# Performance work log

Hardware: AMD Instinct MI355X
Metric: run time of the kernel (lower is better)

## Reference

```python
import jax, jax.numpy as jnp
import numpy as np

B, LQ, C = 4, 4096, 384
NH, NL, NP = 6, 1, 4
HL, WL = 64, 64
LV = HL * WL
DH = C // NH
EPS = 1e-6


def layer_norm(x, g, b):
    mu = jnp.mean(x, axis=-1, keepdims=True)
    var = jnp.mean(jnp.square(x - mu), axis=-1, keepdims=True)
    return (x - mu) * jax.lax.rsqrt(var + EPS) * g + b


def ms_deform_attn_core(value, spatial_shapes, level_start_index, loc, attn_w):
    # value [B,LV,NH,DH]; loc [B,LQ,NH,NL,NP,2] in [0,1]; attn_w [B,LQ,NH,NL,NP]
    ss = np.asarray(spatial_shapes)
    lsi = np.asarray(level_start_index)
    Bv, _, nH, dh = value.shape
    Lq = loc.shape[1]
    nP = loc.shape[4]
    out = jnp.zeros((Bv, Lq, nH, dh), value.dtype)
    for l in range(loc.shape[3]):
        Hl, Wl = int(ss[l, 0]), int(ss[l, 1])
        st = int(lsi[l])
        vflat = value[:, st:st + Hl * Wl]  # [B, Hl*Wl, nH, dh]
        xy = loc[:, :, :, l]               # [B,LQ,nH,NP,2]
        # grid_sample(align_corners=False): pixel = loc * size - 0.5
        x = xy[..., 0] * Wl - 0.5
        y = xy[..., 1] * Hl - 0.5
        x0 = jnp.floor(x)
        y0 = jnp.floor(y)
        wx = x - x0
        wy = y - y0
        x0i = x0.astype(jnp.int32)
        y0i = y0.astype(jnp.int32)

        def gather(xi, yi):
            # zero padding outside the feature map (padding_mode='zeros')
            valid = (xi >= 0) & (xi < Wl) & (yi >= 0) & (yi < Hl)
            idx = jnp.clip(yi, 0, Hl - 1) * Wl + jnp.clip(xi, 0, Wl - 1)  # [B,LQ,nH,NP]
            idx2 = idx.transpose(0, 1, 3, 2).reshape(Bv, Lq * nP, nH)
            g = jnp.take_along_axis(vflat, idx2[..., None], axis=1)       # [B,LQ*NP,nH,dh]
            g = g.reshape(Bv, Lq, nP, nH, dh).transpose(0, 1, 3, 2, 4)    # [B,LQ,nH,NP,dh]
            return g * valid[..., None].astype(value.dtype)

        samp = (gather(x0i, y0i) * ((1 - wx) * (1 - wy))[..., None]
                + gather(x0i + 1, y0i) * (wx * (1 - wy))[..., None]
                + gather(x0i, y0i + 1) * ((1 - wx) * wy)[..., None]
                + gather(x0i + 1, y0i + 1) * (wx * wy)[..., None])
        out = out + jnp.einsum('bqhpd,bqhp->bqhd', samp, attn_w[:, :, :, l])
    return out.reshape(Bv, Lq, nH * dh)


def setup_inputs() -> dict:
    key = jax.random.key(0)
    ks = jax.random.split(key, 12)
    s = 0.02
    return {
        'query': jax.random.normal(ks[0], (B, LQ, C), jnp.float32),
        'reference_points': jax.random.uniform(ks[1], (B, LQ, NL, 2), dtype=jnp.float32),
        'feat': jax.random.normal(ks[2], (B, LV, C), jnp.float32),
        'spatial_shapes': jnp.array([[HL, WL]], jnp.int32),
        'level_start_index': jnp.array([0], jnp.int32),
        'ln_q_g': jnp.ones((C,), jnp.float32), 'ln_q_b': jnp.zeros((C,), jnp.float32),
        'ln_f_g': jnp.ones((C,), jnp.float32), 'ln_f_b': jnp.zeros((C,), jnp.float32),
        'gamma': jax.random.normal(ks[3], (C,), jnp.float32) * 0.1,
        'Wv': jax.random.normal(ks[4], (C, C), jnp.float32) * s,
        'bv': jnp.zeros((C,), jnp.float32),
        'Wo': jax.random.normal(ks[5], (C, NH * NL * NP * 2), jnp.float32) * s,
        'bo': jax.random.normal(ks[6], (NH * NL * NP * 2,), jnp.float32) * 0.5,
        'Wa': jax.random.normal(ks[7], (C, NH * NL * NP), jnp.float32) * s,
        'ba': jnp.zeros((NH * NL * NP,), jnp.float32),
        'Wout': jax.random.normal(ks[8], (C, C), jnp.float32) * s,
        'bout': jnp.zeros((C,), jnp.float32),
    }


def reference(query, reference_points, feat, spatial_shapes, level_start_index,
              ln_q_g, ln_q_b, ln_f_g, ln_f_b, gamma,
              Wv, bv, Wo, bo, Wa, ba, Wout, bout):
    q = layer_norm(query, ln_q_g, ln_q_b)
    f = layer_norm(feat, ln_f_g, ln_f_b)
    value = (f @ Wv + bv).reshape(B, LV, NH, DH)
    offsets = (q @ Wo + bo).reshape(B, LQ, NH, NL, NP, 2)
    attn_w = jax.nn.softmax((q @ Wa + ba).reshape(B, LQ, NH, NL * NP), axis=-1)
    attn_w = attn_w.reshape(B, LQ, NH, NL, NP)
    # offset normalizer is (W, H) per level
    norm = jnp.stack([spatial_shapes[:, 1], spatial_shapes[:, 0]], -1).astype(jnp.float32)
    loc = reference_points[:, :, None, :, None, :] + offsets / norm[None, None, None, :, None, :]
    attn = ms_deform_attn_core(value, spatial_shapes, level_start_index, loc, attn_w)
    attn = attn @ Wout + bout
    return query + gamma * attn
```

## Files before the change

### kernel.cpp

```cpp
#include <hip/hip_runtime.h>
#include <math.h>

#define B_    4
#define LQ_   4096
#define C_    384
#define NH_   6
#define NP_   4
#define HL_   64
#define WL_   64
#define LV_   (HL_ * WL_)
#define ROWS_ (B_ * LQ_)
#define EPS_  1e-6f
#define NOFF_ 48
#define NLOG_ 24
#define WCTR_ 96

typedef unsigned short u16;
typedef unsigned int   u32;
typedef __bf16 bf16x8 __attribute__((ext_vector_type(8)));
typedef float  f32x4  __attribute__((ext_vector_type(4)));

__device__ __forceinline__ u16 f2bf(float f) {
    u32 u = __float_as_uint(f);
    u += 0x7fff + ((u >> 16) & 1);
    return (u16)(u >> 16);
}
__device__ __forceinline__ u32 pack2bf(float a, float b) {
    return (u32)f2bf(a) | ((u32)f2bf(b) << 16);
}

__device__ __forceinline__ f32x4 mfma16(bf16x8 a, bf16x8 b, f32x4 c) {
    return __builtin_amdgcn_mfma_f32_16x16x32_bf16(a, b, c, 0, 0, 0);
}

__device__ __forceinline__ void gl_lds16(const u16* g, u16* l) {
    __builtin_amdgcn_global_load_lds(
        (const __attribute__((address_space(1))) unsigned int*)g,
        (__attribute__((address_space(3))) unsigned int*)l, 16, 0, 0);
}

__device__ __forceinline__ void vm_wait8() { asm volatile("s_waitcnt vmcnt(8)" ::: "memory"); }
__device__ __forceinline__ void vm_wait7() { asm volatile("s_waitcnt vmcnt(7)" ::: "memory"); }
__device__ __forceinline__ void vm_wait6() { asm volatile("s_waitcnt vmcnt(6)" ::: "memory"); }
__device__ __forceinline__ void vm_wait0() { asm volatile("s_waitcnt vmcnt(0)" ::: "memory"); }
__device__ __forceinline__ void lgkm0()    { asm volatile("s_waitcnt lgkmcnt(0)" ::: "memory"); }
__device__ __forceinline__ void barrier_() { asm volatile("s_barrier" ::: "memory"); }

#define LN_BLOCKS_   8192
#define PREP_BLOCKS_ 1297

__global__ __launch_bounds__(256) void ln_prep(
    const float* __restrict__ query, const float* __restrict__ feat,
    const float* __restrict__ qg, const float* __restrict__ qbv,
    const float* __restrict__ fg, const float* __restrict__ fbv,
    u16* __restrict__ qout, u16* __restrict__ fout,
    const float* __restrict__ Wv, const float* __restrict__ Wout,
    const float* __restrict__ Wo, const float* __restrict__ Wa,
    const float* __restrict__ bo, const float* __restrict__ ba,
    u16* __restrict__ WvT, u16* __restrict__ WoutT, u16* __restrict__ WcT,
    float* __restrict__ bias_c)
{
    if (blockIdx.x < LN_BLOCKS_) {
        int wid  = threadIdx.x >> 6;
        int lane = threadIdx.x & 63;
        int row  = blockIdx.x * 4 + wid;
        const float *src, *g, *bsh;
        u16* dst;
        int r;
        if (row < ROWS_) { src = query; g = qg; bsh = qbv; dst = qout; r = row; }
        else             { src = feat;  g = fg; bsh = fbv; dst = fout; r = row - ROWS_; }

        const float* x = src + (size_t)r * C_;
        float4 a4 = *(const float4*)(x + 4 * lane);
        float2 a2 = *(const float2*)(x + 256 + 2 * lane);
        float v0 = a4.x, v1 = a4.y, v2 = a4.z, v3 = a4.w, v4 = a2.x, v5 = a2.y;

        float s = v0 + v1 + v2 + v3 + v4 + v5;
#pragma unroll
        for (int off = 32; off; off >>= 1) s += __shfl_xor(s, off);
        float mu = s * (1.f / C_);

        float d0 = v0 - mu, d1 = v1 - mu, d2 = v2 - mu;
        float d3 = v3 - mu, d4 = v4 - mu, d5 = v5 - mu;
        float s2 = d0*d0 + d1*d1 + d2*d2 + d3*d3 + d4*d4 + d5*d5;
#pragma unroll
        for (int off = 32; off; off >>= 1) s2 += __shfl_xor(s2, off);
        float rs = rsqrtf(s2 * (1.f / C_) + EPS_);

        float4 g4 = *(const float4*)(g + 4 * lane);
        float4 b4 = *(const float4*)(bsh + 4 * lane);
        float2 g2 = *(const float2*)(g + 256 + 2 * lane);
        float2 b2 = *(const float2*)(bsh + 256 + 2 * lane);

        float o0 = d0 * rs * g4.x + b4.x;
        float o1 = d1 * rs * g4.y + b4.y;
        float o2 = d2 * rs * g4.z + b4.z;
        float o3 = d3 * rs * g4.w + b4.w;
        float o4 = d4 * rs * g2.x + b2.x;
        float o5 = d5 * rs * g2.y + b2.y;

        u16* y = dst + (size_t)r * C_;
        uint2 w0; w0.x = pack2bf(o0, o1); w0.y = pack2bf(o2, o3);
        *(uint2*)(y + 4 * lane) = w0;
        *(u32*)(y + 256 + 2 * lane) = pack2bf(o4, o5);
    } else {
        const int KN = 384 * 384;
        int idx = (blockIdx.x - LN_BLOCKS_) * 256 + threadIdx.x;
        if (idx < KN) {
            int n = idx / 384, k = idx - n * 384;
            WvT[idx] = f2bf(Wv[k * 384 + n]);
        } else if (idx < 2 * KN) {
            int t = idx - KN;
            int n = t / 384, k = t - n * 384;
            WoutT[t] = f2bf(Wout[k * 384 + n]);
        } else if (idx < 2 * KN + WCTR_ * 384) {
            int t = idx - 2 * KN;
            int n = t / 384, k = t - n * 384;
            float v = (n < 48) ? Wo[k * 48 + n] : (n < 72 ? Wa[k * 24 + (n - 48)] : 0.f);
            WcT[t] = f2bf(v);
        } else if (idx < 2 * KN + WCTR_ * 384 + 80) {
            int n = idx - (2 * KN + WCTR_ * 384);
            bias_c[n] = (n < 48) ? bo[n] : (n < 72 ? ba[n - 48] : 0.f);
        }
    }
}

__global__ __launch_bounds__(256) void gemm_combined(
    const u16* __restrict__ fb, const u16* __restrict__ qb,
    const u16* __restrict__ WvT, const u16* __restrict__ WcT,
    const float* __restrict__ bv, const float* __restrict__ bias_c,
    u16* __restrict__ valb, float* __restrict__ offs, float* __restrict__ logits)
{
    __shared__ __align__(16) u16 As_[2][8192];
    __shared__ __align__(16) u16 Bs_[2][8192];

    int g    = blockIdx.x;
    int tid  = threadIdx.x;
    int lane = tid & 63, wid = tid >> 6;
    int fr = lane & 15, quad = lane >> 4;

    int swz  = (fr & 7) * 8;
    int off0 = (quad * 8) ^ swz;
    int srow = tid >> 3;
    int csw  = ((tid & 7) ^ (srow & 7)) * 8;

    if (g < 384) {
        int m0 = (g & 127) * 128, n0 = (g >> 7) * 128;
        const u16* aSrc = fb  + (size_t)(m0 + srow) * 384 + csw;
        const u16* bSrc = WvT + (size_t)(n0 + srow) * 384 + csw;

        int wm = (wid >> 1) * 64, wn = (wid & 1) * 64;

        f32x4 zero = {0.f, 0.f, 0.f, 0.f};
        f32x4 acc[4][4];
#pragma unroll
        for (int i = 0; i < 4; ++i)
#pragma unroll
            for (int j = 0; j < 4; ++j) acc[i][j] = zero;

#define STGV(bu, t) { _Pragma("unroll") for (int l = 0; l < 4; ++l) { \
            gl_lds16(aSrc + (size_t)l * (32*384) + (t)*64, &As_[bu][tid*8 + l*2048]); \
            gl_lds16(bSrc + (size_t)l * (32*384) + (t)*64, &Bs_[bu][tid*8 + l*2048]); } }

        STGV(0, 0)
        STGV(1, 1)
#pragma unroll
        for (int t = 0; t < 6; ++t) {
            const int bu = t & 1;
            if (t < 5) vm_wait8(); else vm_wait0();
            barrier_();
            bf16x8 af[4][2], bfr[4][2];
#pragma unroll
            for (int i = 0; i < 4; ++i) {
                int ra = (wm + i * 16 + fr) * 64;
                af[i][0]  = *(const bf16x8*)&As_[bu][ra + off0];
                af[i][1]  = *(const bf16x8*)&As_[bu][ra + (off0 ^ 32)];
                int rb = (wn + i * 16 + fr) * 64;
                bfr[i][0] = *(const bf16x8*)&Bs_[bu][rb + off0];
                bfr[i][1] = *(const bf16x8*)&Bs_[bu][rb + (off0 ^ 32)];
            }
            lgkm0();
            barrier_();
            if (t < 4) STGV(bu, t + 2)
#pragma unroll
            for (int i = 0; i < 4; ++i)
#pragma unroll
                for (int j = 0; j < 4; ++j) {
                    acc[i][j] = mfma16(af[i][0], bfr[j][0], acc[i][j]);
                    acc[i][j] = mfma16(af[i][1], bfr[j][1], acc[i][j]);
                }
        }
#undef STGV

#pragma unroll
        for (int i = 0; i < 4; ++i) {
            int row = m0 + wm + i * 16 + quad * 4;
#pragma unroll
            for (int j = 0; j < 4; ++j) {
                int col = n0 + wn + j * 16 + fr;
                float bcol = bv[col];
#pragma unroll
                for (int r = 0; r < 4; ++r)
                    valb[(size_t)(row + r) * C_ + col] = f2bf(acc[i][j][r] + bcol);
            }
        }
    } else {
        int m0 = (g - 384) * 128;
        const u16* aSrc = qb  + (size_t)(m0 + srow) * 384 + csw;
        const u16* bSrc = WcT + (size_t)srow * 384 + csw;

        int wm = wid * 32;

        f32x4 zero = {0.f, 0.f, 0.f, 0.f};
        f32x4 acc[2][5];
#pragma unroll
        for (int i = 0; i < 2; ++i)
#pragma unroll
            for (int j = 0; j < 5; ++j) acc[i][j] = zero;

#define STGS(bu, t) { _Pragma("unroll") for (int l = 0; l < 4; ++l) \
            gl_lds16(aSrc + (size_t)l * (32*384) + (t)*64, &As_[bu][tid*8 + l*2048]); \
            _Pragma("unroll") for (int l = 0; l < 3; ++l) \
            gl_lds16(bSrc + (size_t)l * (32*384) + (t)*64, &Bs_[bu][tid*8 + l*2048]); }

        STGS(0, 0)
        STGS(1, 1)
#pragma unroll
        for (int t = 0; t < 6; ++t) {
            const int bu = t & 1;
            if (t < 5) vm_wait7(); else vm_wait0();
            barrier_();
            bf16x8 af[2][2], bfr[5][2];
#pragma unroll
            for (int i = 0; i < 2; ++i) {
                int ra = (wm + i * 16 + fr) * 64;
                af[i][0] = *(const bf16x8*)&As_[bu][ra + off0];
                af[i][1] = *(const bf16x8*)&As_[bu][ra + (off0 ^ 32)];
            }
#pragma unroll
            for (int j = 0; j < 5; ++j) {
                int rb = (j * 16 + fr) * 64;
                bfr[j][0] = *(const bf16x8*)&Bs_[bu][rb + off0];
                bfr[j][1] = *(const bf16x8*)&Bs_[bu][rb + (off0 ^ 32)];
            }
            lgkm0();
            barrier_();
            if (t < 4) STGS(bu, t + 2)
#pragma unroll
            for (int i = 0; i < 2; ++i)
#pragma unroll
                for (int j = 0; j < 5; ++j) {
                    acc[i][j] = mfma16(af[i][0], bfr[j][0], acc[i][j]);
                    acc[i][j] = mfma16(af[i][1], bfr[j][1], acc[i][j]);
                }
        }
#undef STGS

#pragma unroll
        for (int i = 0; i < 2; ++i) {
            int row = m0 + wm + i * 16 + quad * 4;
#pragma unroll
            for (int j = 0; j < 5; ++j) {
                int col = j * 16 + fr;
                if (col < 72) {
                    float bcol = bias_c[col];
#pragma unroll
                    for (int r = 0; r < 4; ++r) {
                        float v = acc[i][j][r] + bcol;
                        if (col < 48) offs[(size_t)(row + r) * NOFF_ + col] = v;
                        else          logits[(size_t)(row + r) * NLOG_ + (col - 48)] = v;
                    }
                }
            }
        }
    }
}

__global__ __launch_bounds__(512) void sample_out(
    const u16*  __restrict__ valb,
    const float* __restrict__ rp,
    const float* __restrict__ offs,
    const float* __restrict__ logits,
    const u16* __restrict__ WoutT,
    const float* __restrict__ bout, const float* __restrict__ gamma,
    const float* __restrict__ query, float* __restrict__ out)
{
    __shared__ __align__(16) u16 Al[64 * 384];
    __shared__ __align__(16) u16 Bs_[2][384 * 64];

    int g    = blockIdx.x;
    int tid  = threadIdx.x;
    int lane = tid & 63, wid = tid >> 6;
    int fr = lane & 15, quad = lane >> 4;

    int b     = (g & 7) >> 1;
    int local = ((g >> 3) << 1) | (g & 1);
    int row0  = b * LQ_ + local * 64;

    int srow = tid >> 3;
    int csw  = ((tid & 7) ^ (srow & 7)) * 8;
    const u16* bSrc = WoutT + (size_t)srow * 384 + csw;

#define STGB(bu, t) { _Pragma("unroll") for (int l = 0; l < 6; ++l) \
    gl_lds16(bSrc + (size_t)l * (64*384) + (t)*64, &Bs_[bu][tid*8 + l*4096]); }

    STGB(0, 0)
    STGB(1, 1)

    const u16* vbat = valb + (size_t)b * LV_ * C_;
#pragma unroll
    for (int it = 0; it < 6; ++it) {
        int c   = tid + 512 * it;
        int row = c / 48, dc = c - row * 48;
        int h   = dc >> 3;
        int col0 = dc << 3;
        int r   = row0 + row;

        float4 lg  = *(const float4*)(logits + (size_t)r * NLOG_ + h * 4);
        float2 rpv = *(const float2*)(rp + (size_t)r * 2);
        float4 of0 = *(const float4*)(offs + (size_t)r * NOFF_ + h * 8);
        float4 of1 = *(const float4*)(offs + (size_t)r * NOFF_ + h * 8 + 4);

        float mx = fmaxf(fmaxf(lg.x, lg.y), fmaxf(lg.z, lg.w));
        float e0 = __expf(lg.x - mx), e1 = __expf(lg.y - mx);
        float e2 = __expf(lg.z - mx), e3 = __expf(lg.w - mx);
        float rden = 1.f / (e0 + e1 + e2 + e3);
        float aws[4] = {e0 * rden, e1 * rden, e2 * rden, e3 * rden};
        float oxs[4] = {of0.x, of0.z, of1.x, of1.z};
        float oys[4] = {of0.y, of0.w, of1.y, of1.y};
        oys[3] = of1.w;
        oys[0] = of0.y; oys[1] = of0.w; oys[2] = of1.y;

        const u16* vbase = vbat + col0;
        float acc8[8] = {0.f, 0.f, 0.f, 0.f, 0.f, 0.f, 0.f, 0.f};
#pragma unroll
        for (int p = 0; p < NP_; ++p) {
            float x = rpv.x * (float)WL_ + oxs[p] - 0.5f;
            float y = rpv.y * (float)HL_ + oys[p] - 0.5f;
            float x0f = floorf(x), y0f = floorf(y);
            float wx = x - x0f, wy = y - y0f;
            int x0 = (int)x0f, y0 = (int)y0f;
#pragma unroll
            for (int cc = 0; cc < 4; ++cc) {
                int xi = x0 + (cc & 1);
                int yi = y0 + (cc >> 1);
                bool valid = (xi >= 0) && (xi < WL_) && (yi >= 0) && (yi < HL_);
                int xc = xi < 0 ? 0 : (xi > WL_ - 1 ? WL_ - 1 : xi);
                int yc = yi < 0 ? 0 : (yi > HL_ - 1 ? HL_ - 1 : yi);
                float w = ((cc & 1) ? wx : 1.f - wx) * ((cc >> 1) ? wy : 1.f - wy) * aws[p];
                w = valid ? w : 0.f;
                bf16x8 vv = *(const bf16x8*)(vbase + (size_t)(yc * WL_ + xc) * C_);
#pragma unroll
                for (int e = 0; e < 8; ++e) acc8[e] += w * (float)vv[e];
            }
        }

        uint4 o;
        o.x = pack2bf(acc8[0], acc8[1]);
        o.y = pack2bf(acc8[2], acc8[3]);
        o.z = pack2bf(acc8[4], acc8[5]);
        o.w = pack2bf(acc8[6], acc8[7]);
        *(uint4*)&Al[row * 384 + ((dc ^ (row & 7)) << 3)] = o;
    }
    lgkm0();

    int wn = wid * 48;
    int fs = fr & 7;
    f32x4 zero = {0.f, 0.f, 0.f, 0.f};
    f32x4 acc[4][3];
#pragma unroll
    for (int i = 0; i < 4; ++i)
#pragma unroll
        for (int j = 0; j < 3; ++j) acc[i][j] = zero;

    int off0 = (quad * 8) ^ (fs * 8);

#pragma unroll
    for (int t = 0; t < 6; ++t) {
        const int bu = t & 1;
        if (t < 5) vm_wait6(); else vm_wait0();
        barrier_();
        bf16x8 af[4][2], bfr[3][2];
#pragma unroll
        for (int i = 0; i < 4; ++i) {
            int ra = (i * 16 + fr) * 384;
            af[i][0] = *(const bf16x8*)&Al[ra + (((t * 8 + quad) ^ fs) << 3)];
            af[i][1] = *(const bf16x8*)&Al[ra + (((t * 8 + 4 + quad) ^ fs) << 3)];
        }
#pragma unroll
        for (int j = 0; j < 3; ++j) {
            int rb = (wn + j * 16 + fr) * 64;
            bfr[j][0] = *(const bf16x8*)&Bs_[bu][rb + off0];
            bfr[j][1] = *(const bf16x8*)&Bs_[bu][rb + (off0 ^ 32)];
        }
        lgkm0();
        barrier_();
        if (t < 4) STGB(bu, t + 2)
#pragma unroll
        for (int i = 0; i < 4; ++i)
#pragma unroll
            for (int j = 0; j < 3; ++j) {
                acc[i][j] = mfma16(af[i][0], bfr[j][0], acc[i][j]);
                acc[i][j] = mfma16(af[i][1], bfr[j][1], acc[i][j]);
            }
    }
#undef STGB

#pragma unroll
    for (int i = 0; i < 4; ++i) {
        int rowg = row0 + i * 16 + quad * 4;
#pragma unroll
        for (int j = 0; j < 3; ++j) {
            int col = wn + j * 16 + fr;
            float bc = bout[col], gm = gamma[col];
#pragma unroll
            for (int r = 0; r < 4; ++r) {
                size_t o = (size_t)(rowg + r) * C_ + col;
                out[o] = query[o] + gm * (acc[i][j][r] + bc);
            }
        }
    }
}

extern "C" void kernel_launch(void* const* d_in, const int* in_sizes, int n_in,
                              void* d_out, int out_size, void* d_ws, size_t ws_size,
                              hipStream_t stream)
{
    const float* query  = (const float*)d_in[0];
    const float* rp     = (const float*)d_in[1];
    const float* feat   = (const float*)d_in[2];
    const float* gamma  = (const float*)d_in[9];
    const float* Wv     = (const float*)d_in[10];
    const float* bv     = (const float*)d_in[11];
    const float* Wo     = (const float*)d_in[12];
    const float* bo     = (const float*)d_in[13];
    const float* Wa     = (const float*)d_in[14];
    const float* ba     = (const float*)d_in[15];
    const float* Wout   = (const float*)d_in[16];
    const float* bout   = (const float*)d_in[17];
    float* out = (float*)d_out;

    u16* wsu    = (u16*)d_ws;
    u16* qb     = wsu;
    u16* fb     = qb    + (size_t)ROWS_ * C_;
    u16* valb   = fb    + (size_t)ROWS_ * C_;
    u16* attnb  = valb  + (size_t)ROWS_ * C_;
    u16* WvT    = attnb + (size_t)ROWS_ * C_;
    u16* WoutT  = WvT   + 384 * 384;
    u16* WcT    = WoutT + 384 * 384;
    float* offs   = (float*)(WcT + WCTR_ * 384);
    float* logits = offs + (size_t)ROWS_ * NOFF_;
    float* bias_c = logits + (size_t)ROWS_ * NLOG_;

    ln_prep<<<LN_BLOCKS_ + PREP_BLOCKS_, 256, 0, stream>>>(
        query, feat,
        (const float*)d_in[5], (const float*)d_in[6],
        (const float*)d_in[7], (const float*)d_in[8],
        qb, fb, Wv, Wout, Wo, Wa, bo, ba, WvT, WoutT, WcT, bias_c);

    gemm_combined<<<512, 256, 0, stream>>>(fb, qb, WvT, WcT, bv, bias_c,
                                           valb, offs, logits);

    sample_out<<<256, 512, 0, stream>>>(valb, rp, offs, logits,
                                        WoutT, bout, gamma, query, out);
}
```

Before: 163.9 us.

## Halve sample_out row tile and stream Wout fragments from global into registers

The fused sample+output-projection kernel now handles 32 query rows per block instead of 64, and launches 512 blocks instead of 256. The LDS-staged, double-buffered WoutT tiles are gone. Each wave instead reads its B fragments straight from global/L2 into registers, with a one-step register prefetch across 12 K-steps. This cuts LDS use from roughly 144KB to 24KB, so more blocks can be resident and parallelism rises. In exchange, every block re-reads the Wout slice from cache, and the GEMM now takes more, smaller K iterations.

```diff
diff --git a/kernel.cpp b/kernel.cpp
--- a/kernel.cpp
+++ b/kernel.cpp
@@ -41,7 +41,6 @@
 
 __device__ __forceinline__ void vm_wait8() { asm volatile("s_waitcnt vmcnt(8)" ::: "memory"); }
 __device__ __forceinline__ void vm_wait7() { asm volatile("s_waitcnt vmcnt(7)" ::: "memory"); }
-__device__ __forceinline__ void vm_wait6() { asm volatile("s_waitcnt vmcnt(6)" ::: "memory"); }
 __device__ __forceinline__ void vm_wait0() { asm volatile("s_waitcnt vmcnt(0)" ::: "memory"); }
 __device__ __forceinline__ void lgkm0()    { asm volatile("s_waitcnt lgkmcnt(0)" ::: "memory"); }
 __device__ __forceinline__ void barrier_() { asm volatile("s_barrier" ::: "memory"); }
@@ -285,8 +284,7 @@
     const float* __restrict__ bout, const float* __restrict__ gamma,
     const float* __restrict__ query, float* __restrict__ out)
 {
-    __shared__ __align__(16) u16 Al[64 * 384];
-    __shared__ __align__(16) u16 Bs_[2][384 * 64];
+    __shared__ __align__(16) u16 Al[32 * 384];
 
     int g    = blockIdx.x;
     int tid  = threadIdx.x;
@@ -295,21 +293,11 @@
 
     int b     = (g & 7) >> 1;
     int local = ((g >> 3) << 1) | (g & 1);
-    int row0  = b * LQ_ + local * 64;
-
-    int srow = tid >> 3;
-    int csw  = ((tid & 7) ^ (srow & 7)) * 8;
-    const u16* bSrc = WoutT + (size_t)srow * 384 + csw;
-
-#define STGB(bu, t) { _Pragma("unroll") for (int l = 0; l < 6; ++l) \
-    gl_lds16(bSrc + (size_t)l * (64*384) + (t)*64, &Bs_[bu][tid*8 + l*4096]); }
-
-    STGB(0, 0)
-    STGB(1, 1)
+    int row0  = b * LQ_ + local * 32;
 
     const u16* vbat = valb + (size_t)b * LV_ * C_;
 #pragma unroll
-    for (int it = 0; it < 6; ++it) {
+    for (int it = 0; it < 3; ++it) {
         int c   = tid + 512 * it;
         int row = c / 48, dc = c - row * 48;
         int h   = dc >> 3;
@@ -327,9 +315,7 @@
         float rden = 1.f / (e0 + e1 + e2 + e3);
         float aws[4] = {e0 * rden, e1 * rden, e2 * rden, e3 * rden};
         float oxs[4] = {of0.x, of0.z, of1.x, of1.z};
-        float oys[4] = {of0.y, of0.w, of1.y, of1.y};
-        oys[3] = of1.w;
-        oys[0] = of0.y; oys[1] = of0.w; oys[2] = of1.y;
+        float oys[4] = {of0.y, of0.w, of1.y, of1.w};
 
         const u16* vbase = vbat + col0;
         float acc8[8] = {0.f, 0.f, 0.f, 0.f, 0.f, 0.f, 0.f, 0.f};
@@ -363,51 +349,46 @@
         *(uint4*)&Al[row * 384 + ((dc ^ (row & 7)) << 3)] = o;
     }
     lgkm0();
+    barrier_();
 
     int wn = wid * 48;
     int fs = fr & 7;
     f32x4 zero = {0.f, 0.f, 0.f, 0.f};
-    f32x4 acc[4][3];
-#pragma unroll
-    for (int i = 0; i < 4; ++i)
+    f32x4 acc[2][3];
+#pragma unroll
+    for (int i = 0; i < 2; ++i)
 #pragma unroll
         for (int j = 0; j < 3; ++j) acc[i][j] = zero;
 
-    int off0 = (quad * 8) ^ (fs * 8);
-
-#pragma unroll
-    for (int t = 0; t < 6; ++t) {
-        const int bu = t & 1;
-        if (t < 5) vm_wait6(); else vm_wait0();
-        barrier_();
-        bf16x8 af[4][2], bfr[3][2];
-#pragma unroll
-        for (int i = 0; i < 4; ++i) {
-            int ra = (i * 16 + fr) * 384;
-            af[i][0] = *(const bf16x8*)&Al[ra + (((t * 8 + quad) ^ fs) << 3)];
-            af[i][1] = *(const bf16x8*)&Al[ra + (((t * 8 + 4 + quad) ^ fs) << 3)];
-        }
-#pragma unroll
-        for (int j = 0; j < 3; ++j) {
-            int rb = (wn + j * 16 + fr) * 64;
-            bfr[j][0] = *(const bf16x8*)&Bs_[bu][rb + off0];
-            bfr[j][1] = *(const bf16x8*)&Bs_[bu][rb + (off0 ^ 32)];
-        }
-        lgkm0();
-        barrier_();
-        if (t < 4) STGB(bu, t + 2)
-#pragma unroll
-        for (int i = 0; i < 4; ++i)
-#pragma unroll
-            for (int j = 0; j < 3; ++j) {
-                acc[i][j] = mfma16(af[i][0], bfr[j][0], acc[i][j]);
-                acc[i][j] = mfma16(af[i][1], bfr[j][1], acc[i][j]);
-            }
+    const u16* bBase = WoutT + (size_t)(wn + fr) * 384 + quad * 8;
+    bf16x8 bf[2][3];
+#pragma unroll
+    for (int j = 0; j < 3; ++j)
+        bf[0][j] = *(const bf16x8*)(bBase + (size_t)j * 16 * 384);
+
+#pragma unroll
+    for (int t = 0; t < 12; ++t) {
+        const int cur = t & 1, nxt = cur ^ 1;
+        if (t < 11) {
+#pragma unroll
+            for (int j = 0; j < 3; ++j)
+                bf[nxt][j] = *(const bf16x8*)(bBase + (size_t)j * 16 * 384 + (t + 1) * 32);
+        }
+        bf16x8 af[2];
+#pragma unroll
+        for (int i = 0; i < 2; ++i) {
+            int row = i * 16 + fr;
+            af[i] = *(const bf16x8*)&Al[row * 384 + (((t * 4 + quad) ^ fs) << 3)];
+        }
+#pragma unroll
+        for (int i = 0; i < 2; ++i)
+#pragma unroll
+            for (int j = 0; j < 3; ++j)
+                acc[i][j] = mfma16(af[i], bf[cur][j], acc[i][j]);
     }
-#undef STGB
-
-#pragma unroll
-    for (int i = 0; i < 4; ++i) {
+
+#pragma unroll
+    for (int i = 0; i < 2; ++i) {
         int rowg = row0 + i * 16 + quad * 4;
 #pragma unroll
         for (int j = 0; j < 3; ++j) {
@@ -461,6 +442,6 @@
     gemm_combined<<<512, 256, 0, stream>>>(fb, qb, WvT, WcT, bv, bias_c,
                                            valb, offs, logits);
 
-    sample_out<<<256, 512, 0, stream>>>(valb, rp, offs, logits,
+    sample_out<<<512, 512, 0, stream>>>(valb, rp, offs, logits,
                                         WoutT, bout, gamma, query, out);
 }
```

New measurement: 169.9 us. 3.7% more time.
